# Kernel optimization log

Hardware: AMD Instinct MI355X
Metric: run time of the kernel (lower is better)

## Reference

```python
import jax, jax.numpy as jnp
import numpy as np

N, E, C, D, A, F_, H, RNF = 20000, 200000, 14, 3, 16, 128, 128, 128
CONSTANT = 1.0
LN_EPS = 1e-5


def _pool_matrix(n_channel, dtype):
    ones = np.ones((n_channel, n_channel))
    mats = []
    for i in range(n_channel):
        ws = n_channel - i
        mats.append((np.triu(ones) - np.triu(ones, k=ws)) / ws)
    return jnp.asarray(np.stack(mats), dtype)  # [C, C, C]


def _scatter_mean(src, idx, n):
    s = jax.ops.segment_sum(src, idx, num_segments=n)
    cnt = jax.ops.segment_sum(jnp.ones((src.shape[0],), src.dtype), idx, num_segments=n)
    return s / jnp.maximum(cnt, 1.0).reshape((n,) + (1,) * (src.ndim - 1))


def setup_inputs() -> dict:
    key = jax.random.key(0)
    ks = jax.random.split(key, 24)
    h = jax.random.normal(ks[0], (N, F_), jnp.float32)
    x = jax.random.normal(ks[1], (N, C, D), jnp.float32)
    channel_attr = jax.random.normal(ks[2], (N, C, A), jnp.float32)
    cw = jax.random.uniform(ks[3], (N, C), jnp.float32)
    cw = cw * (jax.random.uniform(ks[4], (N, C)) > 0.3)  # some padded channels
    cw = cw.at[:, 0].set(jax.random.uniform(ks[5], (N,)) + 0.1)  # >=1 valid channel
    row = jax.random.randint(ks[6], (E,), 0, N, dtype=jnp.int32)
    col = jax.random.randint(ks[7], (E,), 0, N, dtype=jnp.int32)

    def lin(k, din, dout):
        return 0.02 * jax.random.normal(k, (din, dout), jnp.float32), jnp.zeros((dout,), jnp.float32)

    rad_w, rad_b = lin(ks[8], A * A, RNF)
    e_w1, e_b1 = lin(ks[9], 2 * F_ + RNF, H)
    e_w2, e_b2 = lin(ks[10], H, H)
    att_w, att_b = lin(ks[11], H, 1)
    c_w1, c_b1 = lin(ks[12], H, H)
    c_w2, c_b2 = lin(ks[13], H, C)
    n_w1, n_b1 = lin(ks[14], F_ + H, H)
    n_w2, n_b2 = lin(ks[15], H, F_)
    ln_g = jnp.ones((F_,), jnp.float32)
    ln_b = jnp.zeros((F_,), jnp.float32)
    return dict(h=h, x=x, channel_attr=channel_attr, channel_weights=cw, row=row, col=col,
                rad_w=rad_w, rad_b=rad_b, e_w1=e_w1, e_b1=e_b1, e_w2=e_w2, e_b2=e_b2,
                att_w=att_w, att_b=att_b, c_w1=c_w1, c_b1=c_b1, c_w2=c_w2, c_b2=c_b2,
                n_w1=n_w1, n_b1=n_b1, n_w2=n_w2, n_b2=n_b2, ln_g=ln_g, ln_b=ln_b)


def reference(h, x, channel_attr, channel_weights, row, col,
              rad_w, rad_b, e_w1, e_b1, e_w2, e_b2, att_w, att_b,
              c_w1, c_b1, c_w2, c_b2, n_w1, n_b1, n_w2, n_b2, ln_g, ln_b):
    silu = jax.nn.silu
    n_nodes = h.shape[0]

    # ---- coord2radial (NUM_SEG = 1) ----
    # pairwise channel distances per edge: [E, C, C]
    coord_msg = jnp.linalg.norm(x[row][:, :, None, :] - x[col][:, None, :, :], axis=-1)
    coord_msg = coord_msg * (channel_weights[row][:, :, None] * channel_weights[col][:, None, :])
    # attr^T @ msg @ attr -> [E, A, A] -> [E, A*A]
    radial = jnp.einsum('eca,ecd,edb->eab', channel_attr[row], coord_msg, channel_attr[col])
    radial = radial.reshape(radial.shape[0], -1)
    radial_norm = jnp.linalg.norm(radial, axis=-1, keepdims=True) + CONSTANT
    radial = (radial @ rad_w + rad_b) / radial_norm

    channel_mask = (channel_weights != 0).astype(x.dtype)  # [N, C]
    channel_sum = jnp.sum(channel_weights != 0, axis=-1).astype(jnp.int32)  # [N]
    pooled_col = (x[col] * channel_mask[col][:, :, None]).sum(1) / channel_sum[col].astype(x.dtype)[:, None]
    coord_diff = x[row] - pooled_col[:, None, :]  # [E, C, 3]

    # ---- edge MLP + attention gate ----
    ef = silu(jnp.concatenate([h[row], h[col], radial], axis=-1) @ e_w1 + e_b1)
    ef = silu(ef @ e_w2 + e_b2)
    ef = ef * jax.nn.sigmoid(ef @ att_w + att_b)  # att_mlp active (hidden_nf == input_nf)

    # ---- RollerPooling on coord_mlp output ----
    cm = silu(ef @ c_w1 + c_b1) @ c_w2 + c_b2  # [E, C]
    pool_mat = _pool_matrix(C, ef.dtype)[channel_sum[row] - 1]  # [E, C, C]
    pooled = jnp.einsum('eij,ej->ei', pool_mat, cm)  # [E, C]
    trans = coord_diff * pooled[:, :, None]  # [E, C, 3]

    x_new = x + _scatter_mean(trans, row, n_nodes)
    agg = _scatter_mean(ef, col, n_nodes)

    nh = silu(jnp.concatenate([h, agg], axis=-1) @ n_w1 + n_b1) @ n_w2 + n_b2
    hr = h + nh
    mu = hr.mean(-1, keepdims=True)
    var = ((hr - mu) ** 2).mean(-1, keepdims=True)
    h_new = (hr - mu) * jax.lax.rsqrt(var + LN_EPS) * ln_g + ln_b
    return h_new, x_new
```

## Files before the change

kernel.cpp:

```cpp
#include <hip/hip_runtime.h>
#include <hip/hip_bf16.h>


#define TE 16
#define TN 16
#define PAD 36

typedef __attribute__((ext_vector_type(8))) short bf16x8;
typedef __attribute__((ext_vector_type(4))) float f32x4;

__device__ __forceinline__ float siluf(float v) { return v / (1.f + __expf(-v)); }
__device__ __forceinline__ float sigmf(float v) { return 1.f / (1.f + __expf(-v)); }
__device__ __forceinline__ short f2bs(float f) {
  union { __hip_bfloat16 b; short s; } u;
  u.b = __float2bfloat16(f);
  return u.s;
}
__device__ __forceinline__ __hip_bfloat162 mk_bf162(float v0, float v1) {
  __hip_bfloat162 r;
  r.x = __float2bfloat16(v0);
  r.y = __float2bfloat16(v1);
  return r;
}

__global__ __launch_bounds__(256) void k_pack(
    const float* __restrict__ h, const float* __restrict__ x,
    const float* __restrict__ attr, const float* __restrict__ cw,
    const float* __restrict__ rad_w, const float* __restrict__ e_w1,
    const float* __restrict__ e_w2, const float* __restrict__ c_w1,
    const float* __restrict__ n_w1, const float* __restrict__ n_w2,
    const float* __restrict__ c_w2,
    __hip_bfloat16* __restrict__ wz_rad, __hip_bfloat16* __restrict__ wz_e1,
    __hip_bfloat16* __restrict__ wz_e2, __hip_bfloat16* __restrict__ wz_c1,
    __hip_bfloat16* __restrict__ wz_n1, __hip_bfloat16* __restrict__ wz_n2,
    __hip_bfloat16* __restrict__ wz_c2,
    __hip_bfloat16* __restrict__ attrS, __hip_bfloat16* __restrict__ hb,
    float* __restrict__ pooled_x, int* __restrict__ chsum, int Nn) {
  int idx = blockIdx.x * 256 + threadIdx.x;
  if (idx < 165888) {
    int i = idx;
    if (i >= 163840) {
      int base = i - 163840;
      int k = base >> 4, n = base & 15;
      wz_c2[(size_t)(k >> 5) * 512 + n * 32 + (k & 31)] =
          (n < 14) ? __float2bfloat16(c_w2[k * 14 + n]) : __float2bfloat16(0.f);
      return;
    }
    const float* W;
    __hip_bfloat16* O;
    int base;
    if (i < 32768) { W = rad_w; O = wz_rad; base = i; }
    else if (i < 81920) { W = e_w1; O = wz_e1; base = i - 32768; }
    else if (i < 98304) { W = e_w2; O = wz_e2; base = i - 81920; }
    else if (i < 114688) { W = c_w1; O = wz_c1; base = i - 98304; }
    else if (i < 147456) { W = n_w1; O = wz_n1; base = i - 114688; }
    else { W = n_w2; O = wz_n2; base = i - 147456; }
    int k = base >> 7, n = base & 127;
    O[(size_t)((k >> 5) * 128 + n) * 32 + (k & 31)] = __float2bfloat16(W[base]);
    return;
  }
  idx -= 165888;
  int na = Nn * 256, nh = Nn * 128;
  if (idx < na) {
    int n = idx >> 8, r = idx & 255, i2 = r >> 4, a = r & 15;
    float v = 0.f;
    if (i2 < 14) v = attr[(size_t)n * 224 + i2 * 16 + a] * cw[(size_t)n * 14 + i2];
    attrS[(size_t)n * 256 + a * 16 + i2] = __float2bfloat16(v);
    return;
  }
  idx -= na;
  if (idx < nh) {
    hb[idx] = __float2bfloat16(h[idx]);
    return;
  }
  idx -= nh;
  if (idx >= Nn) return;
  int n = idx;
  int cnt = 0;
  float sx = 0.f, sy = 0.f, sz = 0.f;
#pragma unroll
  for (int c = 0; c < 14; c++) {
    float w = cw[n * 14 + c];
    if (w != 0.f) {
      cnt++;
      sx += x[n * 42 + c * 3 + 0];
      sy += x[n * 42 + c * 3 + 1];
      sz += x[n * 42 + c * 3 + 2];
    }
  }
  chsum[n] = cnt;
  float inv = 1.f / (float)(cnt > 0 ? cnt : 1);
  pooled_x[n * 3 + 0] = sx * inv;
  pooled_x[n * 3 + 1] = sy * inv;
  pooled_x[n * 3 + 2] = sz * inv;
}

__global__ __launch_bounds__(256, 6) void k_edge(
    const __hip_bfloat16* __restrict__ hb, const float* __restrict__ x,
    const __hip_bfloat16* __restrict__ attrS,
    const int* __restrict__ row, const int* __restrict__ col,
    const float* __restrict__ pooled_x, const int* __restrict__ chsum,
    const __hip_bfloat16* __restrict__ wz_rad, const float* __restrict__ rad_b,
    const __hip_bfloat16* __restrict__ wz_e1, const float* __restrict__ e_b1,
    const __hip_bfloat16* __restrict__ wz_e2, const float* __restrict__ e_b2,
    const float* __restrict__ att_w, const float* __restrict__ att_b,
    const __hip_bfloat16* __restrict__ wz_c1, const float* __restrict__ c_b1,
    const __hip_bfloat16* __restrict__ wz_c2, const float* __restrict__ c_b2,
    unsigned* __restrict__ cnt_row, unsigned* __restrict__ cnt_col,
    __hip_bfloat162* __restrict__ x_acc, __hip_bfloat162* __restrict__ agg, int Ee) {
  __shared__ __hip_bfloat16 sA[12][16][PAD];
  __shared__ __hip_bfloat16 sW[8][16][PAD];
  __shared__ float s_xr[TE][42];
  __shared__ float s_pc[TE][3];
  __shared__ float s_rn[TE];
  __shared__ int s_row[TE], s_col[TE], s_cs[TE];
  float* s_cm   = (float*)&sA[0][0][0];
  float* s_pool = s_cm + 224;
  float* s_red4 = s_pool + 224;
  float* s_att  = s_red4 + 64;

  const int t = threadIdx.x;
  const int e0 = blockIdx.x * TE;
  const int ne = min(TE, Ee - e0);

  if (t < TE) {
    int e = e0 + min(t, ne - 1);
    int r = row[e], c = col[e];
    s_row[t] = r;
    s_col[t] = c;
    s_cs[t] = chsum[r];
    if (t < ne) {
      atomicAdd(&cnt_row[r], 1u);
      atomicAdd(&cnt_col[c], 1u);
    }
  }

  for (int i = t; i < TE * 32; i += 256) {
    int half = i >> 8;
    int m = (i >> 4) & 15, c8 = i & 15;
    int kb = (c8 >> 2) + half * 4, kk = (c8 & 3) * 8;
    int ge = e0 + min(m, ne - 1);
    int node = half ? col[ge] : row[ge];
    *(int4*)&sA[kb][m][kk] = *(const int4*)&hb[(size_t)node * 128 + c8 * 8];
  }
  if (t < TE * 3) {
    int e = t / 3, d = t % 3;
    int ge = e0 + min(e, ne - 1);
    s_pc[e][d] = pooled_x[(size_t)col[ge] * 3 + d];
  }

  const int lane = t & 63, wave = t >> 6, quad = lane >> 4, mr = lane & 15;
  const int n0 = wave * 32;
  const float aw0 = att_w[n0 + mr], aw1 = att_w[n0 + 16 + mr];
  const float att_b0 = att_b[0];

  f32x4 zacc = {0.f, 0.f, 0.f, 0.f};
  const bf16x8 zero8 = {0, 0, 0, 0, 0, 0, 0, 0};

  float xr0v[4], xr1v[4], xr2v[4], xc0v[4], xc1v[4], xc2v[4];
  bf16x8 bCv[4], aRv[4];
#pragma unroll
  for (int p = 0; p < 4; p++) {
    const int e = wave * 4 + p;
    const int ge = e0 + min(e, ne - 1);
    const int re = row[ge], ce = col[ge];
    const int mrc = min(mr, 13);
    const float* xp = x + (size_t)re * 42 + mrc * 3;
    xr0v[p] = xp[0]; xr1v[p] = xp[1]; xr2v[p] = xp[2];
    const float* xq = x + (size_t)ce * 42 + mrc * 3;
    xc0v[p] = xq[0]; xc1v[p] = xq[1]; xc2v[p] = xq[2];
    bCv[p] = zero8; aRv[p] = zero8;
    if (quad < 2) {
      bCv[p] = *(const bf16x8*)&attrS[(size_t)ce * 256 + mr * 16 + quad * 8];
      aRv[p] = *(const bf16x8*)&attrS[(size_t)re * 256 + mr * 16 + quad * 8];
    }
  }
#pragma unroll
  for (int p = 0; p < 4; p++) {
    const int e = wave * 4 + p;
    if (quad == 0 && mr < 14) {
      s_xr[e][mr * 3 + 0] = xr0v[p];
      s_xr[e][mr * 3 + 1] = xr1v[p];
      s_xr[e][mr * 3 + 2] = xr2v[p];
    }
  }

#pragma unroll
  for (int p = 0; p < 4; p++) {
    const int e = wave * 4 + p;
    const float xr0 = xr0v[p], xr1 = xr1v[p], xr2 = xr2v[p];
    const float xc0 = xc0v[p], xc1 = xc1v[p], xc2 = xc2v[p];
    bf16x8 aX = zero8, bX = zero8;
    if (quad == 0) {
      aX[0] = f2bs(xc0); aX[1] = f2bs(xc1); aX[2] = f2bs(xc2);
      bX[0] = f2bs(xr0); bX[1] = f2bs(xr1); bX[2] = f2bs(xr2);
    }
    f32x4 G = __builtin_amdgcn_mfma_f32_16x16x32_bf16(aX, bX, zacc, 0, 0, 0);
    const float nr = xr0 * xr0 + xr1 * xr1 + xr2 * xr2;
    const float nc = xc0 * xc0 + xc1 * xc1 + xc2 * xc2;
    float dD[4];
#pragma unroll
    for (int r = 0; r < 4; r++) {
      float ncj = __shfl(nc, quad * 4 + r);
      dD[r] = sqrtf(fmaxf(ncj + nr - 2.f * G[r], 0.f));
    }
    bf16x8 aD;
#pragma unroll
    for (int jj = 0; jj < 8; jj++) {
      const int qs = (quad * 2 + (jj >> 2)) & 3;
      float dv = __shfl(dD[jj & 3], (qs << 4) | mr);
      if (quad >= 2) dv = 0.f;
      aD[jj] = f2bs(dv);
    }
    f32x4 m1 = __builtin_amdgcn_mfma_f32_16x16x32_bf16(aD, bCv[p], zacc, 0, 0, 0);
    bf16x8 bM;
#pragma unroll
    for (int jj = 0; jj < 8; jj++) {
      const int qs = (quad * 2 + (jj >> 2)) & 3;
      float mv = __shfl(m1[jj & 3], (qs << 4) | mr);
      if (quad >= 2) mv = 0.f;
      bM[jj] = f2bs(mv);
    }
    f32x4 rd = __builtin_amdgcn_mfma_f32_16x16x32_bf16(aRv[p], bM, zacc, 0, 0, 0);
    float ss = rd[0] * rd[0] + rd[1] * rd[1] + rd[2] * rd[2] + rd[3] * rd[3];
    ss += __shfl_xor(ss, 32); ss += __shfl_xor(ss, 16); ss += __shfl_xor(ss, 8);
    ss += __shfl_xor(ss, 4);  ss += __shfl_xor(ss, 2);  ss += __shfl_xor(ss, 1);
    if (lane == 0) s_rn[e] = sqrtf(ss) + 1.0f;
#pragma unroll
    for (int r = 0; r < 4; r++) {
      const int aa = quad * 4 + r;
      sW[aa >> 1][e][((aa & 1) << 4) | mr] = __float2bfloat16(rd[r]);
    }
  }
  __syncthreads();

  {
    f32x4 acc0 = zacc, acc1 = zacc;
#pragma unroll
    for (int kb = 0; kb < 8; kb++) {
      bf16x8 a = *(const bf16x8*)&sW[kb][mr][quad * 8];
      const __hip_bfloat16* wp = wz_rad + ((size_t)(kb * 128 + n0 + mr) * 32 + quad * 8);
      bf16x8 b0 = *(const bf16x8*)wp;
      bf16x8 b1 = *(const bf16x8*)(wp + 16 * 32);
      acc0 = __builtin_amdgcn_mfma_f32_16x16x32_bf16(a, b0, acc0, 0, 0, 0);
      acc1 = __builtin_amdgcn_mfma_f32_16x16x32_bf16(a, b1, acc1, 0, 0, 0);
    }
    float bias0 = rad_b[n0 + mr], bias1 = rad_b[n0 + 16 + mr];
#pragma unroll
    for (int r = 0; r < 4; r++) {
      int e = quad * 4 + r;
      float inv = 1.f / s_rn[e];
      sA[8 + wave][e][mr]      = __float2bfloat16((acc0[r] + bias0) * inv);
      sA[8 + wave][e][16 + mr] = __float2bfloat16((acc1[r] + bias1) * inv);
    }
  }
  __syncthreads();
  {
    f32x4 acc0 = zacc, acc1 = zacc;
#pragma unroll
    for (int kb = 0; kb < 12; kb++) {
      bf16x8 a = *(const bf16x8*)&sA[kb][mr][quad * 8];
      const __hip_bfloat16* wp = wz_e1 + ((size_t)(kb * 128 + n0 + mr) * 32 + quad * 8);
      bf16x8 b0 = *(const bf16x8*)wp;
      bf16x8 b1 = *(const bf16x8*)(wp + 16 * 32);
      acc0 = __builtin_amdgcn_mfma_f32_16x16x32_bf16(a, b0, acc0, 0, 0, 0);
      acc1 = __builtin_amdgcn_mfma_f32_16x16x32_bf16(a, b1, acc1, 0, 0, 0);
    }
    float bias0 = e_b1[n0 + mr], bias1 = e_b1[n0 + 16 + mr];
#pragma unroll
    for (int r = 0; r < 4; r++) {
      int e = quad * 4 + r;
      sW[wave][e][mr]      = __float2bfloat16(siluf(acc0[r] + bias0));
      sW[wave][e][16 + mr] = __float2bfloat16(siluf(acc1[r] + bias1));
    }
  }
  __syncthreads();
  {
    f32x4 acc0 = zacc, acc1 = zacc;
#pragma unroll
    for (int kb = 0; kb < 4; kb++) {
      bf16x8 a = *(const bf16x8*)&sW[kb][mr][quad * 8];
      const __hip_bfloat16* wp = wz_e2 + ((size_t)(kb * 128 + n0 + mr) * 32 + quad * 8);
      bf16x8 b0 = *(const bf16x8*)wp;
      bf16x8 b1 = *(const bf16x8*)(wp + 16 * 32);
      acc0 = __builtin_amdgcn_mfma_f32_16x16x32_bf16(a, b0, acc0, 0, 0, 0);
      acc1 = __builtin_amdgcn_mfma_f32_16x16x32_bf16(a, b1, acc1, 0, 0, 0);
    }
    float bias0 = e_b2[n0 + mr], bias1 = e_b2[n0 + 16 + mr];
    float part[4];
#pragma unroll
    for (int r = 0; r < 4; r++) {
      int e = quad * 4 + r;
      float v0 = siluf(acc0[r] + bias0);
      float v1 = siluf(acc1[r] + bias1);
      sW[4 + wave][e][mr]      = __float2bfloat16(v0);
      sW[4 + wave][e][16 + mr] = __float2bfloat16(v1);
      part[r] = v0 * aw0 + v1 * aw1;
    }
#pragma unroll
    for (int msk = 1; msk < 16; msk <<= 1) {
#pragma unroll
      for (int r = 0; r < 4; r++) part[r] += __shfl_xor(part[r], msk);
    }
    if (mr == 0) {
#pragma unroll
      for (int r = 0; r < 4; r++) s_red4[wave * 16 + quad * 4 + r] = part[r];
    }
  }
  __syncthreads();
  if (t < TE) {
    float s = s_red4[t] + s_red4[16 + t] + s_red4[32 + t] + s_red4[48 + t];
    s_att[t] = sigmf(s + att_b0);
  }
  __syncthreads();
  {
    f32x4 acc0 = zacc, acc1 = zacc;
#pragma unroll
    for (int kb = 0; kb < 4; kb++) {
      bf16x8 a = *(const bf16x8*)&sW[4 + kb][mr][quad * 8];
      const __hip_bfloat16* wp = wz_c1 + ((size_t)(kb * 128 + n0 + mr) * 32 + quad * 8);
      bf16x8 b0 = *(const bf16x8*)wp;
      bf16x8 b1 = *(const bf16x8*)(wp + 16 * 32);
      acc0 = __builtin_amdgcn_mfma_f32_16x16x32_bf16(a, b0, acc0, 0, 0, 0);
      acc1 = __builtin_amdgcn_mfma_f32_16x16x32_bf16(a, b1, acc1, 0, 0, 0);
    }
    float bias0 = c_b1[n0 + mr], bias1 = c_b1[n0 + 16 + mr];
#pragma unroll
    for (int r = 0; r < 4; r++) {
      int e = quad * 4 + r;
      float av = s_att[e];
      sW[wave][e][mr]      = __float2bfloat16(siluf(av * acc0[r] + bias0));
      sW[wave][e][16 + mr] = __float2bfloat16(siluf(av * acc1[r] + bias1));
    }
  }
  __syncthreads();
  if (wave == 0) {
    f32x4 acc = zacc;
#pragma unroll
    for (int kb = 0; kb < 4; kb++) {
      bf16x8 a = *(const bf16x8*)&sW[kb][mr][quad * 8];
      bf16x8 b = *(const bf16x8*)(wz_c2 + ((size_t)(kb * 16 + mr) * 32 + quad * 8));
      acc = __builtin_amdgcn_mfma_f32_16x16x32_bf16(a, b, acc, 0, 0, 0);
    }
    if (mr < 14) {
      float bias = c_b2[mr];
#pragma unroll
      for (int r = 0; r < 4; r++) s_cm[(quad * 4 + r) * 14 + mr] = acc[r] + bias;
    }
  }
  __syncthreads();
  if (t < TE * 14) {
    int e = t / 14, c = t % 14;
    int wsz = 15 - s_cs[e];
    int hi = min(c + wsz, 14);
    float s = 0.f;
    for (int j = c; j < hi; j++) s += s_cm[e * 14 + j];
    s_pool[e * 14 + c] = s / (float)wsz;
  }
  __syncthreads();
  for (int i = t; i < TE * 21; i += 256) {
    int e = i / 21, pr = i % 21;
    if (e < ne) {
      int r0 = pr * 2, r1 = r0 + 1;
      float v0 = (s_xr[e][r0] - s_pc[e][r0 % 3]) * s_pool[e * 14 + r0 / 3];
      float v1 = (s_xr[e][r1] - s_pc[e][r1 % 3]) * s_pool[e * 14 + r1 / 3];
      unsafeAtomicAdd(&x_acc[(size_t)s_row[e] * 21 + pr], mk_bf162(v0, v1));
    }
  }
  for (int i = t; i < TE * 64; i += 256) {
    int e = i >> 6, o2 = i & 63;
    if (e < ne) {
      float av = s_att[e];
      const __hip_bfloat16* wp2 = &sW[4 + (o2 >> 4)][e][(o2 & 15) * 2];
      float v0 = __bfloat162float(wp2[0]) * av;
      float v1 = __bfloat162float(wp2[1]) * av;
      unsafeAtomicAdd(&agg[(size_t)s_col[e] * 64 + o2], mk_bf162(v0, v1));
    }
  }
}

__global__ __launch_bounds__(256) void k_node(
    const float* __restrict__ h, const __hip_bfloat162* __restrict__ agg,
    const unsigned* __restrict__ cnt_col,
    const __hip_bfloat16* __restrict__ wz_n1, const float* __restrict__ n_b1,
    const __hip_bfloat16* __restrict__ wz_n2, const float* __restrict__ n_b2,
    const float* __restrict__ ln_g, const float* __restrict__ ln_b,
    const float* __restrict__ x, const __hip_bfloat162* __restrict__ x_acc,
    const unsigned* __restrict__ cnt_row,
    float* __restrict__ out_h, float* __restrict__ out_x, int Nn) {
  __shared__ __hip_bfloat16 sA[8][16][PAD];
  __shared__ __hip_bfloat16 sT[4][16][PAD];
  __shared__ float s_h[TN][128];
  __shared__ float s_o[TN][132];
  const int t = threadIdx.x;
  const int nb0 = blockIdx.x * TN;
  const int nn = min(TN, Nn - nb0);

  for (int i = t; i < TN * 21; i += 256) {
    int n = i / 21, pr = i % 21;
    if (n < nn) {
      int gn = nb0 + n;
      unsigned c = cnt_row[gn];
      float inv = 1.f / (float)(c > 0 ? c : 1);
      float2 xa = __bfloat1622float2(x_acc[(size_t)gn * 21 + pr]);
      size_t gi = (size_t)gn * 42 + pr * 2;
      out_x[gi]     = x[gi] + xa.x * inv;
      out_x[gi + 1] = x[gi + 1] + xa.y * inv;
    }
  }

  for (int i = t; i < TN * 64; i += 256) {
    int m = i >> 6, kp = (i & 63) << 1;
    int kb = kp >> 5, kk = kp & 31;
    int gn = nb0 + min(m, nn - 1);
    const float2 hv = *(const float2*)&h[(size_t)gn * 128 + kp];
    sA[kb][m][kk]     = __float2bfloat16(hv.x);
    sA[kb][m][kk + 1] = __float2bfloat16(hv.y);
    s_h[m][kp]     = hv.x;
    s_h[m][kp + 1] = hv.y;
    unsigned c = cnt_col[gn];
    float inv = 1.f / (float)(c > 0 ? c : 1);
    float2 gv = __bfloat1622float2(agg[(size_t)gn * 64 + (kp >> 1)]);
    sA[4 + kb][m][kk]     = __float2bfloat16(gv.x * inv);
    sA[4 + kb][m][kk + 1] = __float2bfloat16(gv.y * inv);
  }
  __syncthreads();
  const int lane = t & 63, wave = t >> 6, quad = lane >> 4, mr = lane & 15;
  const int n0 = wave * 32;
  f32x4 zacc = {0.f, 0.f, 0.f, 0.f};
  {
    f32x4 acc0 = zacc, acc1 = zacc;
#pragma unroll
    for (int kb = 0; kb < 8; kb++) {
      bf16x8 a = *(const bf16x8*)&sA[kb][mr][quad * 8];
      const __hip_bfloat16* wp = wz_n1 + ((size_t)(kb * 128 + n0 + mr) * 32 + quad * 8);
      bf16x8 b0 = *(const bf16x8*)wp;
      bf16x8 b1 = *(const bf16x8*)(wp + 16 * 32);
      acc0 = __builtin_amdgcn_mfma_f32_16x16x32_bf16(a, b0, acc0, 0, 0, 0);
      acc1 = __builtin_amdgcn_mfma_f32_16x16x32_bf16(a, b1, acc1, 0, 0, 0);
    }
    float bias0 = n_b1[n0 + mr], bias1 = n_b1[n0 + 16 + mr];
#pragma unroll
    for (int r = 0; r < 4; r++) {
      int m = quad * 4 + r;
      sT[wave][m][mr]      = __float2bfloat16(siluf(acc0[r] + bias0));
      sT[wave][m][16 + mr] = __float2bfloat16(siluf(acc1[r] + bias1));
    }
  }
  __syncthreads();
  {
    f32x4 acc0 = zacc, acc1 = zacc;
#pragma unroll
    for (int kb = 0; kb < 4; kb++) {
      bf16x8 a = *(const bf16x8*)&sT[kb][mr][quad * 8];
      const __hip_bfloat16* wp = wz_n2 + ((size_t)(kb * 128 + n0 + mr) * 32 + quad * 8);
      bf16x8 b0 = *(const bf16x8*)wp;
      bf16x8 b1 = *(const bf16x8*)(wp + 16 * 32);
      acc0 = __builtin_amdgcn_mfma_f32_16x16x32_bf16(a, b0, acc0, 0, 0, 0);
      acc1 = __builtin_amdgcn_mfma_f32_16x16x32_bf16(a, b1, acc1, 0, 0, 0);
    }
    float bias0 = n_b2[n0 + mr], bias1 = n_b2[n0 + 16 + mr];
#pragma unroll
    for (int r = 0; r < 4; r++) {
      int m = quad * 4 + r;
      s_o[m][n0 + mr]      = s_h[m][n0 + mr] + acc0[r] + bias0;
      s_o[m][n0 + 16 + mr] = s_h[m][n0 + 16 + mr] + acc1[r] + bias1;
    }
  }
  __syncthreads();
  {
    int n = t >> 4, p = t & 15;
    float v[8];
    float s = 0.f;
#pragma unroll
    for (int j = 0; j < 8; j++) {
      v[j] = s_o[n][p * 8 + j];
      s += v[j];
    }
    s += __shfl_xor(s, 1); s += __shfl_xor(s, 2);
    s += __shfl_xor(s, 4); s += __shfl_xor(s, 8);
    float mu = s * (1.f / 128.f);
    float var = 0.f;
#pragma unroll
    for (int j = 0; j < 8; j++) {
      float d = v[j] - mu;
      var += d * d;
    }
    var += __shfl_xor(var, 1); var += __shfl_xor(var, 2);
    var += __shfl_xor(var, 4); var += __shfl_xor(var, 8);
    float rs = rsqrtf(var * (1.f / 128.f) + 1e-5f);
    if (n < nn) {
      size_t base = (size_t)(nb0 + n) * 128 + p * 8;
#pragma unroll
      for (int j = 0; j < 8; j++)
        out_h[base + j] = (v[j] - mu) * rs * ln_g[p * 8 + j] + ln_b[p * 8 + j];
    }
  }
}

extern "C" void kernel_launch(void* const* d_in, const int* in_sizes, int n_in,
                              void* d_out, int out_size, void* d_ws, size_t ws_size,
                              hipStream_t stream) {
  const float* h     = (const float*)d_in[0];
  const float* x     = (const float*)d_in[1];
  const float* attr  = (const float*)d_in[2];
  const float* cw    = (const float*)d_in[3];
  const int*   row   = (const int*)d_in[4];
  const int*   col   = (const int*)d_in[5];
  const float* rad_w = (const float*)d_in[6];
  const float* rad_b = (const float*)d_in[7];
  const float* e_w1  = (const float*)d_in[8];
  const float* e_b1  = (const float*)d_in[9];
  const float* e_w2  = (const float*)d_in[10];
  const float* e_b2  = (const float*)d_in[11];
  const float* att_w = (const float*)d_in[12];
  const float* att_b = (const float*)d_in[13];
  const float* c_w1  = (const float*)d_in[14];
  const float* c_b1  = (const float*)d_in[15];
  const float* c_w2  = (const float*)d_in[16];
  const float* c_b2  = (const float*)d_in[17];
  const float* n_w1  = (const float*)d_in[18];
  const float* n_b1  = (const float*)d_in[19];
  const float* n_w2  = (const float*)d_in[20];
  const float* n_b2  = (const float*)d_in[21];
  const float* ln_g  = (const float*)d_in[22];
  const float* ln_b  = (const float*)d_in[23];

  const int N = in_sizes[0] / 128;
  const int E = in_sizes[4];

  char* ws = (char*)d_ws;
  size_t off = 0;
  auto alloc = [&](size_t bytes) {
    size_t o = off;
    off += (bytes + 255) & ~(size_t)255;
    return o;
  };
  size_t off_wzr  = alloc(32768 * sizeof(__hip_bfloat16));
  size_t off_wz1  = alloc(49152 * sizeof(__hip_bfloat16));
  size_t off_wz2  = alloc(16384 * sizeof(__hip_bfloat16));
  size_t off_wzc  = alloc(16384 * sizeof(__hip_bfloat16));
  size_t off_wzn1 = alloc(32768 * sizeof(__hip_bfloat16));
  size_t off_wzn2 = alloc(16384 * sizeof(__hip_bfloat16));
  size_t off_wzc2 = alloc(2048 * sizeof(__hip_bfloat16));
  size_t off_atS  = alloc((size_t)N * 256 * sizeof(__hip_bfloat16));
  size_t off_hb   = alloc((size_t)N * 128 * sizeof(__hip_bfloat16));
  size_t off_px   = alloc((size_t)N * 3 * sizeof(float));
  size_t off_cs   = alloc((size_t)N * sizeof(int));
  size_t off_cntr = alloc((size_t)N * sizeof(unsigned));
  size_t off_cntc = alloc((size_t)N * sizeof(unsigned));
  size_t off_xacc = alloc((size_t)N * 21 * sizeof(__hip_bfloat162));
  size_t off_agg  = alloc((size_t)N * 64 * sizeof(__hip_bfloat162));

  __hip_bfloat16* wz_rad = (__hip_bfloat16*)(ws + off_wzr);
  __hip_bfloat16* wz_e1  = (__hip_bfloat16*)(ws + off_wz1);
  __hip_bfloat16* wz_e2  = (__hip_bfloat16*)(ws + off_wz2);
  __hip_bfloat16* wz_c1  = (__hip_bfloat16*)(ws + off_wzc);
  __hip_bfloat16* wz_n1  = (__hip_bfloat16*)(ws + off_wzn1);
  __hip_bfloat16* wz_n2  = (__hip_bfloat16*)(ws + off_wzn2);
  __hip_bfloat16* wz_c2  = (__hip_bfloat16*)(ws + off_wzc2);
  __hip_bfloat16* attrS  = (__hip_bfloat16*)(ws + off_atS);
  __hip_bfloat16* hb     = (__hip_bfloat16*)(ws + off_hb);
  float* pooled_x   = (float*)(ws + off_px);
  int* chsum        = (int*)(ws + off_cs);
  unsigned* cnt_row = (unsigned*)(ws + off_cntr);
  unsigned* cnt_col = (unsigned*)(ws + off_cntc);
  __hip_bfloat162* x_acc = (__hip_bfloat162*)(ws + off_xacc);
  __hip_bfloat162* agg   = (__hip_bfloat162*)(ws + off_agg);

  (void)hipMemsetAsync(ws + off_cntr, 0, off - off_cntr, stream);

  const int pack_items = 165888 + N * 256 + N * 128 + N;
  k_pack<<<dim3((pack_items + 255) / 256), dim3(256), 0, stream>>>(
      h, x, attr, cw, rad_w, e_w1, e_w2, c_w1, n_w1, n_w2, c_w2,
      wz_rad, wz_e1, wz_e2, wz_c1, wz_n1, wz_n2, wz_c2,
      attrS, hb, pooled_x, chsum, N);
  k_edge<<<dim3((E + TE - 1) / TE), dim3(256), 0, stream>>>(
      hb, x, attrS, row, col, pooled_x, chsum,
      wz_rad, rad_b, wz_e1, e_b1, wz_e2, e_b2, att_w, att_b,
      wz_c1, c_b1, wz_c2, c_b2, cnt_row, cnt_col, x_acc, agg, E);
  k_node<<<dim3((N + TN - 1) / TN), dim3(256), 0, stream>>>(
      h, agg, cnt_col, wz_n1, n_b1, wz_n2, n_b2, ln_g, ln_b,
      x, x_acc, cnt_row, (float*)d_out, (float*)d_out + (size_t)N * 128, N);
}
```

Before: 396.3 us.

## Split edge kernel into radial stage and 64-edge-tile MLP stage

Splits the fused edge kernel in two. The first kernel computes the radial features per 16-edge tile and writes them to a bf16 global buffer of shape E×128. The second runs the edge MLP, attention, coord MLP and scatters over 64-edge tiles, so each weight fragment loaded from global memory is reused across four MFMA row-fragments instead of one. The cost is an extra launch plus a 51 MB write and read of the intermediate radial features, and x and pooled_x are now read from global memory during the scatter.

```diff
diff --git a/kernel.cpp b/kernel.cpp
--- a/kernel.cpp
+++ b/kernel.cpp
@@ -3,6 +3,7 @@
 
 
 #define TE 16
+#define TM 64
 #define TN 16
 #define PAD 36
 
@@ -95,65 +96,26 @@
   pooled_x[n * 3 + 2] = sz * inv;
 }
 
-__global__ __launch_bounds__(256, 6) void k_edge(
-    const __hip_bfloat16* __restrict__ hb, const float* __restrict__ x,
-    const __hip_bfloat16* __restrict__ attrS,
+__global__ __launch_bounds__(256) void k_rad(
+    const float* __restrict__ x, const __hip_bfloat16* __restrict__ attrS,
     const int* __restrict__ row, const int* __restrict__ col,
-    const float* __restrict__ pooled_x, const int* __restrict__ chsum,
     const __hip_bfloat16* __restrict__ wz_rad, const float* __restrict__ rad_b,
-    const __hip_bfloat16* __restrict__ wz_e1, const float* __restrict__ e_b1,
-    const __hip_bfloat16* __restrict__ wz_e2, const float* __restrict__ e_b2,
-    const float* __restrict__ att_w, const float* __restrict__ att_b,
-    const __hip_bfloat16* __restrict__ wz_c1, const float* __restrict__ c_b1,
-    const __hip_bfloat16* __restrict__ wz_c2, const float* __restrict__ c_b2,
     unsigned* __restrict__ cnt_row, unsigned* __restrict__ cnt_col,
-    __hip_bfloat162* __restrict__ x_acc, __hip_bfloat162* __restrict__ agg, int Ee) {
-  __shared__ __hip_bfloat16 sA[12][16][PAD];
+    __hip_bfloat16* __restrict__ radf, int Ee) {
   __shared__ __hip_bfloat16 sW[8][16][PAD];
-  __shared__ float s_xr[TE][42];
-  __shared__ float s_pc[TE][3];
   __shared__ float s_rn[TE];
-  __shared__ int s_row[TE], s_col[TE], s_cs[TE];
-  float* s_cm   = (float*)&sA[0][0][0];
-  float* s_pool = s_cm + 224;
-  float* s_red4 = s_pool + 224;
-  float* s_att  = s_red4 + 64;
 
   const int t = threadIdx.x;
   const int e0 = blockIdx.x * TE;
   const int ne = min(TE, Ee - e0);
 
-  if (t < TE) {
-    int e = e0 + min(t, ne - 1);
-    int r = row[e], c = col[e];
-    s_row[t] = r;
-    s_col[t] = c;
-    s_cs[t] = chsum[r];
-    if (t < ne) {
-      atomicAdd(&cnt_row[r], 1u);
-      atomicAdd(&cnt_col[c], 1u);
-    }
-  }
-
-  for (int i = t; i < TE * 32; i += 256) {
-    int half = i >> 8;
-    int m = (i >> 4) & 15, c8 = i & 15;
-    int kb = (c8 >> 2) + half * 4, kk = (c8 & 3) * 8;
-    int ge = e0 + min(m, ne - 1);
-    int node = half ? col[ge] : row[ge];
-    *(int4*)&sA[kb][m][kk] = *(const int4*)&hb[(size_t)node * 128 + c8 * 8];
-  }
-  if (t < TE * 3) {
-    int e = t / 3, d = t % 3;
-    int ge = e0 + min(e, ne - 1);
-    s_pc[e][d] = pooled_x[(size_t)col[ge] * 3 + d];
+  if (t < ne) {
+    atomicAdd(&cnt_row[row[e0 + t]], 1u);
+    atomicAdd(&cnt_col[col[e0 + t]], 1u);
   }
 
   const int lane = t & 63, wave = t >> 6, quad = lane >> 4, mr = lane & 15;
   const int n0 = wave * 32;
-  const float aw0 = att_w[n0 + mr], aw1 = att_w[n0 + 16 + mr];
-  const float att_b0 = att_b[0];
-
   f32x4 zacc = {0.f, 0.f, 0.f, 0.f};
   const bf16x8 zero8 = {0, 0, 0, 0, 0, 0, 0, 0};
 
@@ -175,15 +137,6 @@
       aRv[p] = *(const bf16x8*)&attrS[(size_t)re * 256 + mr * 16 + quad * 8];
     }
   }
-#pragma unroll
-  for (int p = 0; p < 4; p++) {
-    const int e = wave * 4 + p;
-    if (quad == 0 && mr < 14) {
-      s_xr[e][mr * 3 + 0] = xr0v[p];
-      s_xr[e][mr * 3 + 1] = xr1v[p];
-      s_xr[e][mr * 3 + 2] = xr2v[p];
-    }
-  }
 
 #pragma unroll
   for (int p = 0; p < 4; p++) {
@@ -249,108 +202,194 @@
 #pragma unroll
     for (int r = 0; r < 4; r++) {
       int e = quad * 4 + r;
-      float inv = 1.f / s_rn[e];
-      sA[8 + wave][e][mr]      = __float2bfloat16((acc0[r] + bias0) * inv);
-      sA[8 + wave][e][16 + mr] = __float2bfloat16((acc1[r] + bias1) * inv);
-    }
-  }
-  __syncthreads();
-  {
-    f32x4 acc0 = zacc, acc1 = zacc;
+      if (e < ne) {
+        float inv = 1.f / s_rn[e];
+        size_t base = (size_t)(e0 + e) * 128;
+        radf[base + n0 + mr]      = __float2bfloat16((acc0[r] + bias0) * inv);
+        radf[base + n0 + 16 + mr] = __float2bfloat16((acc1[r] + bias1) * inv);
+      }
+    }
+  }
+}
+
+__global__ __launch_bounds__(256, 2) void k_mlp(
+    const __hip_bfloat16* __restrict__ hb, const __hip_bfloat16* __restrict__ radf,
+    const float* __restrict__ x, const float* __restrict__ pooled_x,
+    const int* __restrict__ row, const int* __restrict__ col,
+    const int* __restrict__ chsum,
+    const __hip_bfloat16* __restrict__ wz_e1, const float* __restrict__ e_b1,
+    const __hip_bfloat16* __restrict__ wz_e2, const float* __restrict__ e_b2,
+    const float* __restrict__ att_w, const float* __restrict__ att_b,
+    const __hip_bfloat16* __restrict__ wz_c1, const float* __restrict__ c_b1,
+    const __hip_bfloat16* __restrict__ wz_c2, const float* __restrict__ c_b2,
+    __hip_bfloat162* __restrict__ x_acc, __hip_bfloat162* __restrict__ agg,
+    int Ee) {
+  __shared__ __hip_bfloat16 sA[12][TM][PAD];
+  __shared__ __hip_bfloat16 sE1[4][TM][PAD];
+  __shared__ float s_att[TM];
+  __shared__ float s_red[4][TM];
+  __shared__ int s_row[TM], s_col[TM], s_cs[TM];
+  float* s_cm = (float*)&sA[8][0][0];
+  float* s_pool = (float*)&sA[10][0][0];
+
+  const int t = threadIdx.x;
+  const int e0 = blockIdx.x * TM;
+  const int ne = min(TM, Ee - e0);
+
+  if (t < TM) {
+    int ge = e0 + min(t, ne - 1);
+    int r = row[ge];
+    s_row[t] = r;
+    s_col[t] = col[ge];
+    s_cs[t] = chsum[r];
+  }
+  __syncthreads();
+
+  {
+    const int m = t >> 2, part = t & 3;
+    const __hip_bfloat16* hr = hb + (size_t)s_row[m] * 128 + part * 8;
+    const __hip_bfloat16* hc = hb + (size_t)s_col[m] * 128 + part * 8;
+    const __hip_bfloat16* rf = radf + (size_t)(e0 + min(m, ne - 1)) * 128 + part * 8;
+#pragma unroll
+    for (int kb = 0; kb < 4; kb++) {
+      *(int4*)&sA[kb][m][part * 8]     = *(const int4*)&hr[kb * 32];
+      *(int4*)&sA[4 + kb][m][part * 8] = *(const int4*)&hc[kb * 32];
+      *(int4*)&sA[8 + kb][m][part * 8] = *(const int4*)&rf[kb * 32];
+    }
+  }
+  __syncthreads();
+
+  const int lane = t & 63, wave = t >> 6, quad = lane >> 4, mr = lane & 15;
+  const int n0 = wave * 32;
+  const f32x4 zacc = {0.f, 0.f, 0.f, 0.f};
+
+  {
+    f32x4 a0[4], a1[4];
+#pragma unroll
+    for (int mf = 0; mf < 4; mf++) { a0[mf] = zacc; a1[mf] = zacc; }
 #pragma unroll
     for (int kb = 0; kb < 12; kb++) {
-      bf16x8 a = *(const bf16x8*)&sA[kb][mr][quad * 8];
       const __hip_bfloat16* wp = wz_e1 + ((size_t)(kb * 128 + n0 + mr) * 32 + quad * 8);
       bf16x8 b0 = *(const bf16x8*)wp;
       bf16x8 b1 = *(const bf16x8*)(wp + 16 * 32);
-      acc0 = __builtin_amdgcn_mfma_f32_16x16x32_bf16(a, b0, acc0, 0, 0, 0);
-      acc1 = __builtin_amdgcn_mfma_f32_16x16x32_bf16(a, b1, acc1, 0, 0, 0);
+#pragma unroll
+      for (int mf = 0; mf < 4; mf++) {
+        bf16x8 a = *(const bf16x8*)&sA[kb][mf * 16 + mr][quad * 8];
+        a0[mf] = __builtin_amdgcn_mfma_f32_16x16x32_bf16(a, b0, a0[mf], 0, 0, 0);
+        a1[mf] = __builtin_amdgcn_mfma_f32_16x16x32_bf16(a, b1, a1[mf], 0, 0, 0);
+      }
     }
     float bias0 = e_b1[n0 + mr], bias1 = e_b1[n0 + 16 + mr];
 #pragma unroll
-    for (int r = 0; r < 4; r++) {
-      int e = quad * 4 + r;
-      sW[wave][e][mr]      = __float2bfloat16(siluf(acc0[r] + bias0));
-      sW[wave][e][16 + mr] = __float2bfloat16(siluf(acc1[r] + bias1));
-    }
-  }
-  __syncthreads();
-  {
-    f32x4 acc0 = zacc, acc1 = zacc;
+    for (int mf = 0; mf < 4; mf++)
+#pragma unroll
+      for (int r = 0; r < 4; r++) {
+        int e = mf * 16 + quad * 4 + r;
+        sE1[wave][e][mr]      = __float2bfloat16(siluf(a0[mf][r] + bias0));
+        sE1[wave][e][16 + mr] = __float2bfloat16(siluf(a1[mf][r] + bias1));
+      }
+  }
+  __syncthreads();
+
+  const float aw0 = att_w[n0 + mr], aw1 = att_w[n0 + 16 + mr];
+  {
+    f32x4 a0[4], a1[4];
+#pragma unroll
+    for (int mf = 0; mf < 4; mf++) { a0[mf] = zacc; a1[mf] = zacc; }
 #pragma unroll
     for (int kb = 0; kb < 4; kb++) {
-      bf16x8 a = *(const bf16x8*)&sW[kb][mr][quad * 8];
       const __hip_bfloat16* wp = wz_e2 + ((size_t)(kb * 128 + n0 + mr) * 32 + quad * 8);
       bf16x8 b0 = *(const bf16x8*)wp;
       bf16x8 b1 = *(const bf16x8*)(wp + 16 * 32);
-      acc0 = __builtin_amdgcn_mfma_f32_16x16x32_bf16(a, b0, acc0, 0, 0, 0);
-      acc1 = __builtin_amdgcn_mfma_f32_16x16x32_bf16(a, b1, acc1, 0, 0, 0);
+#pragma unroll
+      for (int mf = 0; mf < 4; mf++) {
+        bf16x8 a = *(const bf16x8*)&sE1[kb][mf * 16 + mr][quad * 8];
+        a0[mf] = __builtin_amdgcn_mfma_f32_16x16x32_bf16(a, b0, a0[mf], 0, 0, 0);
+        a1[mf] = __builtin_amdgcn_mfma_f32_16x16x32_bf16(a, b1, a1[mf], 0, 0, 0);
+      }
     }
     float bias0 = e_b2[n0 + mr], bias1 = e_b2[n0 + 16 + mr];
-    float part[4];
-#pragma unroll
-    for (int r = 0; r < 4; r++) {
-      int e = quad * 4 + r;
-      float v0 = siluf(acc0[r] + bias0);
-      float v1 = siluf(acc1[r] + bias1);
-      sW[4 + wave][e][mr]      = __float2bfloat16(v0);
-      sW[4 + wave][e][16 + mr] = __float2bfloat16(v1);
-      part[r] = v0 * aw0 + v1 * aw1;
-    }
-#pragma unroll
-    for (int msk = 1; msk < 16; msk <<= 1) {
-#pragma unroll
-      for (int r = 0; r < 4; r++) part[r] += __shfl_xor(part[r], msk);
-    }
+    float part[4][4];
+#pragma unroll
+    for (int mf = 0; mf < 4; mf++)
+#pragma unroll
+      for (int r = 0; r < 4; r++) {
+        int e = mf * 16 + quad * 4 + r;
+        float v0 = siluf(a0[mf][r] + bias0);
+        float v1 = siluf(a1[mf][r] + bias1);
+        sA[wave][e][mr]      = __float2bfloat16(v0);
+        sA[wave][e][16 + mr] = __float2bfloat16(v1);
+        part[mf][r] = v0 * aw0 + v1 * aw1;
+      }
+#pragma unroll
+    for (int msk = 1; msk < 16; msk <<= 1)
+#pragma unroll
+      for (int mf = 0; mf < 4; mf++)
+#pragma unroll
+        for (int r = 0; r < 4; r++) part[mf][r] += __shfl_xor(part[mf][r], msk);
     if (mr == 0) {
 #pragma unroll
-      for (int r = 0; r < 4; r++) s_red4[wave * 16 + quad * 4 + r] = part[r];
-    }
-  }
-  __syncthreads();
-  if (t < TE) {
-    float s = s_red4[t] + s_red4[16 + t] + s_red4[32 + t] + s_red4[48 + t];
-    s_att[t] = sigmf(s + att_b0);
-  }
-  __syncthreads();
-  {
-    f32x4 acc0 = zacc, acc1 = zacc;
+      for (int mf = 0; mf < 4; mf++)
+#pragma unroll
+        for (int r = 0; r < 4; r++)
+          s_red[wave][mf * 16 + quad * 4 + r] = part[mf][r];
+    }
+  }
+  __syncthreads();
+  if (t < TM) {
+    float s = s_red[0][t] + s_red[1][t] + s_red[2][t] + s_red[3][t];
+    s_att[t] = sigmf(s + att_b[0]);
+  }
+  __syncthreads();
+
+  {
+    f32x4 a0[4], a1[4];
+#pragma unroll
+    for (int mf = 0; mf < 4; mf++) { a0[mf] = zacc; a1[mf] = zacc; }
 #pragma unroll
     for (int kb = 0; kb < 4; kb++) {
-      bf16x8 a = *(const bf16x8*)&sW[4 + kb][mr][quad * 8];
       const __hip_bfloat16* wp = wz_c1 + ((size_t)(kb * 128 + n0 + mr) * 32 + quad * 8);
       bf16x8 b0 = *(const bf16x8*)wp;
       bf16x8 b1 = *(const bf16x8*)(wp + 16 * 32);
-      acc0 = __builtin_amdgcn_mfma_f32_16x16x32_bf16(a, b0, acc0, 0, 0, 0);
-      acc1 = __builtin_amdgcn_mfma_f32_16x16x32_bf16(a, b1, acc1, 0, 0, 0);
+#pragma unroll
+      for (int mf = 0; mf < 4; mf++) {
+        bf16x8 a = *(const bf16x8*)&sA[kb][mf * 16 + mr][quad * 8];
+        a0[mf] = __builtin_amdgcn_mfma_f32_16x16x32_bf16(a, b0, a0[mf], 0, 0, 0);
+        a1[mf] = __builtin_amdgcn_mfma_f32_16x16x32_bf16(a, b1, a1[mf], 0, 0, 0);
+      }
     }
     float bias0 = c_b1[n0 + mr], bias1 = c_b1[n0 + 16 + mr];
 #pragma unroll
-    for (int r = 0; r < 4; r++) {
-      int e = quad * 4 + r;
-      float av = s_att[e];
-      sW[wave][e][mr]      = __float2bfloat16(siluf(av * acc0[r] + bias0));
-      sW[wave][e][16 + mr] = __float2bfloat16(siluf(av * acc1[r] + bias1));
-    }
-  }
-  __syncthreads();
-  if (wave == 0) {
+    for (int mf = 0; mf < 4; mf++)
+#pragma unroll
+      for (int r = 0; r < 4; r++) {
+        int e = mf * 16 + quad * 4 + r;
+        float av = s_att[e];
+        sA[4 + wave][e][mr]      = __float2bfloat16(siluf(av * a0[mf][r] + bias0));
+        sA[4 + wave][e][16 + mr] = __float2bfloat16(siluf(av * a1[mf][r] + bias1));
+      }
+  }
+  __syncthreads();
+
+  {
     f32x4 acc = zacc;
 #pragma unroll
     for (int kb = 0; kb < 4; kb++) {
-      bf16x8 a = *(const bf16x8*)&sW[kb][mr][quad * 8];
+      bf16x8 a = *(const bf16x8*)&sA[4 + kb][wave * 16 + mr][quad * 8];
       bf16x8 b = *(const bf16x8*)(wz_c2 + ((size_t)(kb * 16 + mr) * 32 + quad * 8));
       acc = __builtin_amdgcn_mfma_f32_16x16x32_bf16(a, b, acc, 0, 0, 0);
     }
     if (mr < 14) {
       float bias = c_b2[mr];
 #pragma unroll
-      for (int r = 0; r < 4; r++) s_cm[(quad * 4 + r) * 14 + mr] = acc[r] + bias;
-    }
-  }
-  __syncthreads();
-  if (t < TE * 14) {
-    int e = t / 14, c = t % 14;
+      for (int r = 0; r < 4; r++)
+        s_cm[(wave * 16 + quad * 4 + r) * 14 + mr] = acc[r] + bias;
+    }
+  }
+  __syncthreads();
+
+  for (int i = t; i < TM * 14; i += 256) {
+    int e = i / 14, c = i % 14;
     int wsz = 15 - s_cs[e];
     int hi = min(c + wsz, 14);
     float s = 0.f;
@@ -358,20 +397,23 @@
     s_pool[e * 14 + c] = s / (float)wsz;
   }
   __syncthreads();
-  for (int i = t; i < TE * 21; i += 256) {
+
+  for (int i = t; i < TM * 21; i += 256) {
     int e = i / 21, pr = i % 21;
     if (e < ne) {
       int r0 = pr * 2, r1 = r0 + 1;
-      float v0 = (s_xr[e][r0] - s_pc[e][r0 % 3]) * s_pool[e * 14 + r0 / 3];
-      float v1 = (s_xr[e][r1] - s_pc[e][r1 % 3]) * s_pool[e * 14 + r1 / 3];
+      const float* xp = x + (size_t)s_row[e] * 42;
+      const float* pc = pooled_x + (size_t)s_col[e] * 3;
+      float v0 = (xp[r0] - pc[r0 % 3]) * s_pool[e * 14 + r0 / 3];
+      float v1 = (xp[r1] - pc[r1 % 3]) * s_pool[e * 14 + r1 / 3];
       unsafeAtomicAdd(&x_acc[(size_t)s_row[e] * 21 + pr], mk_bf162(v0, v1));
     }
   }
-  for (int i = t; i < TE * 64; i += 256) {
+  for (int i = t; i < TM * 64; i += 256) {
     int e = i >> 6, o2 = i & 63;
     if (e < ne) {
       float av = s_att[e];
-      const __hip_bfloat16* wp2 = &sW[4 + (o2 >> 4)][e][(o2 & 15) * 2];
+      const __hip_bfloat16* wp2 = &sA[o2 >> 4][e][(o2 & 15) * 2];
       float v0 = __bfloat162float(wp2[0]) * av;
       float v1 = __bfloat162float(wp2[1]) * av;
       unsafeAtomicAdd(&agg[(size_t)s_col[e] * 64 + o2], mk_bf162(v0, v1));
@@ -545,6 +587,7 @@
   size_t off_wzc2 = alloc(2048 * sizeof(__hip_bfloat16));
   size_t off_atS  = alloc((size_t)N * 256 * sizeof(__hip_bfloat16));
   size_t off_hb   = alloc((size_t)N * 128 * sizeof(__hip_bfloat16));
+  size_t off_radf = alloc((size_t)E * 128 * sizeof(__hip_bfloat16));
   size_t off_px   = alloc((size_t)N * 3 * sizeof(float));
   size_t off_cs   = alloc((size_t)N * sizeof(int));
   size_t off_cntr = alloc((size_t)N * sizeof(unsigned));
@@ -561,6 +604,7 @@
   __hip_bfloat16* wz_c2  = (__hip_bfloat16*)(ws + off_wzc2);
   __hip_bfloat16* attrS  = (__hip_bfloat16*)(ws + off_atS);
   __hip_bfloat16* hb     = (__hip_bfloat16*)(ws + off_hb);
+  __hip_bfloat16* radf   = (__hip_bfloat16*)(ws + off_radf);
   float* pooled_x   = (float*)(ws + off_px);
   int* chsum        = (int*)(ws + off_cs);
   unsigned* cnt_row = (unsigned*)(ws + off_cntr);
@@ -575,10 +619,12 @@
       h, x, attr, cw, rad_w, e_w1, e_w2, c_w1, n_w1, n_w2, c_w2,
       wz_rad, wz_e1, wz_e2, wz_c1, wz_n1, wz_n2, wz_c2,
       attrS, hb, pooled_x, chsum, N);
-  k_edge<<<dim3((E + TE - 1) / TE), dim3(256), 0, stream>>>(
-      hb, x, attrS, row, col, pooled_x, chsum,
-      wz_rad, rad_b, wz_e1, e_b1, wz_e2, e_b2, att_w, att_b,
-      wz_c1, c_b1, wz_c2, c_b2, cnt_row, cnt_col, x_acc, agg, E);
+  k_rad<<<dim3((E + TE - 1) / TE), dim3(256), 0, stream>>>(
+      x, attrS, row, col, wz_rad, rad_b, cnt_row, cnt_col, radf, E);
+  k_mlp<<<dim3((E + TM - 1) / TM), dim3(256), 0, stream>>>(
+      hb, radf, x, pooled_x, row, col, chsum,
+      wz_e1, e_b1, wz_e2, e_b2, att_w, att_b,
+      wz_c1, c_b1, wz_c2, c_b2, x_acc, agg, E);
   k_node<<<dim3((N + TN - 1) / TN), dim3(256), 0, stream>>>(
       h, agg, cnt_col, wz_n1, n_b1, wz_n2, n_b2, ln_g, ln_b,
       x, x_acc, cnt_row, (float*)d_out, (float*)d_out + (size_t)N * 128, N);
```

After: 418.5 us. +5.6%, slower.
